# Kernel optimization log

Hardware: AMD Instinct MI355X
Metric: run time of the kernel (lower is better)

Reference implementation:

```python
import jax, jax.numpy as jnp
import numpy as np

B, N, F = 256, 131072, 8


def setup_inputs() -> dict:
    key = jax.random.key(0)
    k1, k2 = jax.random.split(key)
    x = jax.random.normal(k1, (B, N), dtype=jnp.float32)
    # keras 'random_normal' initializer uses stddev=0.05; also keeps the IIR stable
    w = jax.random.normal(k2, (F,), dtype=jnp.float32) * 0.05
    return {"x": x, "w": w}


def reference(x, w):
    # Causal IIR recurrence:
    #   v[i] = 0                                   for i < F
    #   v[i] = x[i] + sum_{j=0}^{F-1} w[j] * v[i-j-1]   for i >= F
    # carry[:, j] holds v[i-1-j] for each batch row.
    Bx, Nx = x.shape
    Fw = w.shape[0]

    def step(carry, inp):
        xt, active = inp                      # xt: [B], active: scalar bool
        v = jnp.where(active, xt + carry @ w, jnp.zeros_like(xt))  # [B]
        new_carry = jnp.concatenate([v[:, None], carry[:, :-1]], axis=1)
        return new_carry, v

    carry0 = jnp.zeros((Bx, Fw), dtype=x.dtype)
    active = jnp.arange(Nx) >= Fw            # v[i]=0 until i >= filter_size
    _, ys = jax.lax.scan(step, carry0, (x.T, active))  # ys: [N, B]
    return ys.T                               # [B, N]
```

## Files before the change

### kernel.cpp

```cpp
#include <hip/hip_runtime.h>


constexpr int Bn   = 256;
constexpr int Nn   = 131072;
constexpr int Lc   = 32;
constexpr int Kn   = 64;
constexpr int TPB  = 256;
constexpr int SPAN = TPB * Lc;
constexpr int TROW = Nn / SPAN;
constexpr int PAD  = 36;

typedef float f32x4 __attribute__((ext_vector_type(4)));

#define IIR_STEP(vv, xx, a0,a1,a2,a3,a4,a5,a6,a7)                             \
    vv = fmaf(w0,(a0), fmaf(w1,(a1), fmaf(w2,(a2), fmaf(w3,(a3),              \
         fmaf(w4,(a4), fmaf(w5,(a5), fmaf(w6,(a6), fmaf(w7,(a7), (xx)))))))))

#define IIR_GROUP8(xa, xb)                                                    \
    IIR_STEP(v0, (xa).x, s0,s1,s2,s3,s4,s5,s6,s7);                            \
    IIR_STEP(v1, (xa).y, v0,s0,s1,s2,s3,s4,s5,s6);                            \
    IIR_STEP(v2, (xa).z, v1,v0,s0,s1,s2,s3,s4,s5);                            \
    IIR_STEP(v3, (xa).w, v2,v1,v0,s0,s1,s2,s3,s4);                            \
    IIR_STEP(v4, (xb).x, v3,v2,v1,v0,s0,s1,s2,s3);                            \
    IIR_STEP(v5, (xb).y, v4,v3,v2,v1,v0,s0,s1,s2);                            \
    IIR_STEP(v6, (xb).z, v5,v4,v3,v2,v1,v0,s0,s1);                            \
    IIR_STEP(v7, (xb).w, v6,v5,v4,v3,v2,v1,v0,s0);                            \
    s0=v7; s1=v6; s2=v5; s3=v4; s4=v3; s5=v2; s6=v1; s7=v0;

__global__ __launch_bounds__(256, 4)
void iir_kernel(const float* __restrict__ x,
                const float* __restrict__ wp,
                float* __restrict__ out) {
    __shared__ float tile[TPB * PAD];

    const int t = threadIdx.x;
    const int b = blockIdx.x;
    const size_t base = (size_t)b * SPAN;
    const bool row_start = ((b & (TROW - 1)) == 0);

    const float w0 = wp[0], w1 = wp[1], w2 = wp[2], w3 = wp[3],
                w4 = wp[4], w5 = wp[5], w6 = wp[6], w7 = wp[7];

    #pragma unroll
    for (int k = 0; k < 8; ++k) {
        const int f   = k * TPB + t;
        const float4 v = *reinterpret_cast<const float4*>(x + base + 4 * (size_t)f);
        const int c   = f >> 3;
        const int off = (f & 7) * 4;
        *reinterpret_cast<float4*>(&tile[c * PAD + off]) = v;
    }
    __syncthreads();

    float s0=0.f,s1=0.f,s2=0.f,s3=0.f,s4=0.f,s5=0.f,s6=0.f,s7=0.f;
    const int p = t * Lc;

    if (row_start && t == 0) {
    } else if (row_start && t < 3) {
        for (int e = 8; e < p; e += 8) {
            const float* lq = &tile[(e >> 5) * PAD + (e & 31)];
            float4 xa = *reinterpret_cast<const float4*>(lq);
            float4 xb = *reinterpret_cast<const float4*>(lq + 4);
            float v0,v1,v2,v3,v4,v5,v6,v7;
            IIR_GROUP8(xa, xb);
        }
    } else if (!row_start && t < 2) {
        const float* g = x + base + p - Kn;
        #pragma unroll
        for (int m = 0; m < Kn / 8; ++m) {
            float4 xa = *reinterpret_cast<const float4*>(g + 8 * m);
            float4 xb = *reinterpret_cast<const float4*>(g + 8 * m + 4);
            float v0,v1,v2,v3,v4,v5,v6,v7;
            IIR_GROUP8(xa, xb);
        }
    } else {
        const float* lq0 = &tile[(t - 2) * PAD];
        #pragma unroll
        for (int m = 0; m < 8; ++m) {
            const float* lq = lq0 + (m >> 2) * PAD + (m & 3) * 8;
            float4 xa = *reinterpret_cast<const float4*>(lq);
            float4 xb = *reinterpret_cast<const float4*>(lq + 4);
            float v0,v1,v2,v3,v4,v5,v6,v7;
            IIR_GROUP8(xa, xb);
        }
    }
    __syncthreads();

    {
        float* lp = &tile[t * PAD];
        if (row_start && t == 0) {
            *reinterpret_cast<float4*>(lp)     = make_float4(0.f,0.f,0.f,0.f);
            *reinterpret_cast<float4*>(lp + 4) = make_float4(0.f,0.f,0.f,0.f);
            #pragma unroll
            for (int gi = 1; gi < 4; ++gi) {
                float* q = lp + gi * 8;
                float4 xa = *reinterpret_cast<const float4*>(q);
                float4 xb = *reinterpret_cast<const float4*>(q + 4);
                float v0,v1,v2,v3,v4,v5,v6,v7;
                IIR_GROUP8(xa, xb);
                *reinterpret_cast<float4*>(q)     = make_float4(v0,v1,v2,v3);
                *reinterpret_cast<float4*>(q + 4) = make_float4(v4,v5,v6,v7);
            }
        } else {
            #pragma unroll
            for (int gi = 0; gi < 4; ++gi) {
                float* q = lp + gi * 8;
                float4 xa = *reinterpret_cast<const float4*>(q);
                float4 xb = *reinterpret_cast<const float4*>(q + 4);
                float v0,v1,v2,v3,v4,v5,v6,v7;
                IIR_GROUP8(xa, xb);
                *reinterpret_cast<float4*>(q)     = make_float4(v0,v1,v2,v3);
                *reinterpret_cast<float4*>(q + 4) = make_float4(v4,v5,v6,v7);
            }
        }
    }
    __syncthreads();

    #pragma unroll
    for (int k = 0; k < 8; ++k) {
        const int f   = k * TPB + t;
        const int c   = f >> 3;
        const int off = (f & 7) * 4;
        const f32x4 v = *reinterpret_cast<const f32x4*>(&tile[c * PAD + off]);
        __builtin_nontemporal_store(v, reinterpret_cast<f32x4*>(out + base + 4 * (size_t)f));
    }
}

extern "C" void kernel_launch(void* const* d_in, const int* in_sizes, int n_in,
                              void* d_out, int out_size, void* d_ws, size_t ws_size,
                              hipStream_t stream) {
    const float* x = (const float*)d_in[0];
    const float* w = (const float*)d_in[1];
    float* out     = (float*)d_out;

    const int grid = (Bn * Nn) / SPAN;
    iir_kernel<<<grid, TPB, 0, stream>>>(x, w, out);
}
```

Before: 53.11 us.

## Load input tile directly into LDS with XOR swizzle instead of padding

Replaces the register-staged global-to-LDS copy with global_load_lds direct loads, permuting the global source addresses so the LDS layout follows an XOR swizzle rather than a padded stride. All LDS accesses move to the swizzled indexing, which shrinks shared memory to the unpadded size. The launch-bounds occupancy hint rises from 4 to 5 blocks. The aim is to cut VGPR traffic and LDS footprint for higher occupancy and more overlap, at the cost of trickier addressing that has to match the per-wave LDS write pattern of the direct-load instruction.

```diff
diff --git a/kernel.cpp b/kernel.cpp
--- a/kernel.cpp
+++ b/kernel.cpp
@@ -8,9 +8,12 @@
 constexpr int TPB  = 256;
 constexpr int SPAN = TPB * Lc;
 constexpr int TROW = Nn / SPAN;
-constexpr int PAD  = 36;
 
 typedef float f32x4 __attribute__((ext_vector_type(4)));
+
+__device__ __forceinline__ int swz(int c, int o) {
+    return c * 32 + ((o ^ (c & 7)) << 2);
+}
 
 #define IIR_STEP(vv, xx, a0,a1,a2,a3,a4,a5,a6,a7)                             \
     vv = fmaf(w0,(a0), fmaf(w1,(a1), fmaf(w2,(a2), fmaf(w3,(a3),              \
@@ -27,11 +30,11 @@
     IIR_STEP(v7, (xb).w, v6,v5,v4,v3,v2,v1,v0,s0);                            \
     s0=v7; s1=v6; s2=v5; s3=v4; s4=v3; s5=v2; s6=v1; s7=v0;
 
-__global__ __launch_bounds__(256, 4)
+__global__ __launch_bounds__(256, 5)
 void iir_kernel(const float* __restrict__ x,
                 const float* __restrict__ wp,
                 float* __restrict__ out) {
-    __shared__ float tile[TPB * PAD];
+    __shared__ float tile[TPB * Lc];
 
     const int t = threadIdx.x;
     const int b = blockIdx.x;
@@ -41,13 +44,19 @@
     const float w0 = wp[0], w1 = wp[1], w2 = wp[2], w3 = wp[3],
                 w4 = wp[4], w5 = wp[5], w6 = wp[6], w7 = wp[7];
 
-    #pragma unroll
-    for (int k = 0; k < 8; ++k) {
-        const int f   = k * TPB + t;
-        const float4 v = *reinterpret_cast<const float4*>(x + base + 4 * (size_t)f);
-        const int c   = f >> 3;
-        const int off = (f & 7) * 4;
-        *reinterpret_cast<float4*>(&tile[c * PAD + off]) = v;
+    {
+        const char* gx = (const char*)(x + base);
+        #pragma unroll
+        for (int k = 0; k < 8; ++k) {
+            const int s  = k * TPB + t;
+            const int gi = s ^ ((s >> 3) & 7);
+            const void* gsrc = gx + (size_t)gi * 16;
+            float* lbase = &tile[(k * TPB + (t & ~63)) * 4];
+            __builtin_amdgcn_global_load_lds(
+                (const __attribute__((address_space(1))) void*)gsrc,
+                (__attribute__((address_space(3))) void*)lbase,
+                16, 0, 0);
+        }
     }
     __syncthreads();
 
@@ -57,9 +66,9 @@
     if (row_start && t == 0) {
     } else if (row_start && t < 3) {
         for (int e = 8; e < p; e += 8) {
-            const float* lq = &tile[(e >> 5) * PAD + (e & 31)];
-            float4 xa = *reinterpret_cast<const float4*>(lq);
-            float4 xb = *reinterpret_cast<const float4*>(lq + 4);
+            const int c = e >> 5, g = (e & 31) >> 2;
+            const f32x4 xa = *reinterpret_cast<const f32x4*>(&tile[swz(c, g)]);
+            const f32x4 xb = *reinterpret_cast<const f32x4*>(&tile[swz(c, g + 1)]);
             float v0,v1,v2,v3,v4,v5,v6,v7;
             IIR_GROUP8(xa, xb);
         }
@@ -73,55 +82,46 @@
             IIR_GROUP8(xa, xb);
         }
     } else {
-        const float* lq0 = &tile[(t - 2) * PAD];
         #pragma unroll
-        for (int m = 0; m < 8; ++m) {
-            const float* lq = lq0 + (m >> 2) * PAD + (m & 3) * 8;
-            float4 xa = *reinterpret_cast<const float4*>(lq);
-            float4 xb = *reinterpret_cast<const float4*>(lq + 4);
-            float v0,v1,v2,v3,v4,v5,v6,v7;
-            IIR_GROUP8(xa, xb);
+        for (int cc = 0; cc < 2; ++cc) {
+            const int c = t - 2 + cc;
+            #pragma unroll
+            for (int m = 0; m < 4; ++m) {
+                const f32x4 xa = *reinterpret_cast<const f32x4*>(&tile[swz(c, 2*m)]);
+                const f32x4 xb = *reinterpret_cast<const f32x4*>(&tile[swz(c, 2*m + 1)]);
+                float v0,v1,v2,v3,v4,v5,v6,v7;
+                IIR_GROUP8(xa, xb);
+            }
         }
     }
     __syncthreads();
 
     {
-        float* lp = &tile[t * PAD];
+        int gstart = 0;
         if (row_start && t == 0) {
-            *reinterpret_cast<float4*>(lp)     = make_float4(0.f,0.f,0.f,0.f);
-            *reinterpret_cast<float4*>(lp + 4) = make_float4(0.f,0.f,0.f,0.f);
-            #pragma unroll
-            for (int gi = 1; gi < 4; ++gi) {
-                float* q = lp + gi * 8;
-                float4 xa = *reinterpret_cast<const float4*>(q);
-                float4 xb = *reinterpret_cast<const float4*>(q + 4);
-                float v0,v1,v2,v3,v4,v5,v6,v7;
-                IIR_GROUP8(xa, xb);
-                *reinterpret_cast<float4*>(q)     = make_float4(v0,v1,v2,v3);
-                *reinterpret_cast<float4*>(q + 4) = make_float4(v4,v5,v6,v7);
-            }
-        } else {
-            #pragma unroll
-            for (int gi = 0; gi < 4; ++gi) {
-                float* q = lp + gi * 8;
-                float4 xa = *reinterpret_cast<const float4*>(q);
-                float4 xb = *reinterpret_cast<const float4*>(q + 4);
-                float v0,v1,v2,v3,v4,v5,v6,v7;
-                IIR_GROUP8(xa, xb);
-                *reinterpret_cast<float4*>(q)     = make_float4(v0,v1,v2,v3);
-                *reinterpret_cast<float4*>(q + 4) = make_float4(v4,v5,v6,v7);
-            }
+            *reinterpret_cast<f32x4*>(&tile[swz(0,0)]) = (f32x4){0.f,0.f,0.f,0.f};
+            *reinterpret_cast<f32x4*>(&tile[swz(0,1)]) = (f32x4){0.f,0.f,0.f,0.f};
+            gstart = 1;
+        }
+        for (int gi = gstart; gi < 4; ++gi) {
+            f32x4* qa = reinterpret_cast<f32x4*>(&tile[swz(t, 2*gi)]);
+            f32x4* qb = reinterpret_cast<f32x4*>(&tile[swz(t, 2*gi + 1)]);
+            const f32x4 xa = *qa;
+            const f32x4 xb = *qb;
+            float v0,v1,v2,v3,v4,v5,v6,v7;
+            IIR_GROUP8(xa, xb);
+            *qa = (f32x4){v0, v1, v2, v3};
+            *qb = (f32x4){v4, v5, v6, v7};
         }
     }
     __syncthreads();
 
     #pragma unroll
     for (int k = 0; k < 8; ++k) {
-        const int f   = k * TPB + t;
-        const int c   = f >> 3;
-        const int off = (f & 7) * 4;
-        const f32x4 v = *reinterpret_cast<const f32x4*>(&tile[c * PAD + off]);
-        __builtin_nontemporal_store(v, reinterpret_cast<f32x4*>(out + base + 4 * (size_t)f));
+        const int s = k * TPB + t;
+        const int c = s >> 3, o = s & 7;
+        const f32x4 v = *reinterpret_cast<const f32x4*>(&tile[swz(c, o)]);
+        __builtin_nontemporal_store(v, reinterpret_cast<f32x4*>(out + base + 4 * (size_t)s));
     }
 }
 
```

Result: slower. 56.99 us (+7.3%).
